# Optimization experiments

Measured on AMD Instinct MI355X. Metric: run time of the kernel, lower is better.

Reference implementation:

```python
import jax, jax.numpy as jnp
import numpy as np

B, T, C = 4, 2048, 1024
NH = 16
HD = C // NH
ROPE_BASE = 10000.0


def setup_inputs() -> dict:
    key = jax.random.key(0)
    k1, k2, k3, k4, k5 = jax.random.split(key, 5)
    s = 1.0 / np.sqrt(C)
    return {
        "x": jax.random.normal(k1, (B, T, C), dtype=jnp.float32),
        "W_qkv": jax.random.normal(k2, (C, 3 * C), dtype=jnp.float32) * s,
        "b_qkv": jax.random.normal(k3, (3 * C,), dtype=jnp.float32) * 0.02,
        "W_proj": jax.random.normal(k4, (C, C), dtype=jnp.float32) * s,
        "b_proj": jax.random.normal(k5, (C,), dtype=jnp.float32) * 0.02,
    }


def _rotate_half(u):
    u1, u2 = u[..., : HD // 2], u[..., HD // 2 :]
    return jnp.concatenate((-u2, u1), axis=-1)


def _rope_cos_sin(t, dtype):
    # inv_freq: [HD/2]; positions: [T]
    inv_freq = 1.0 / (ROPE_BASE ** (jnp.arange(0, HD, 2, dtype=jnp.float32) / HD))
    pos = jnp.arange(t, dtype=jnp.float32)
    freqs = pos[:, None] * inv_freq[None, :]          # [T, HD/2]
    emb = jnp.concatenate((freqs, freqs), axis=-1)    # [T, HD]
    return jnp.cos(emb).astype(dtype), jnp.sin(emb).astype(dtype)


def reference(x, W_qkv, b_qkv, W_proj, b_proj):
    b, t, c = x.shape
    qkv = x @ W_qkv + b_qkv                           # [B,T,3C]
    q, k, v = jnp.split(qkv, 3, axis=-1)
    # [B,T,C] -> [B,NH,T,HD]
    def to_heads(u):
        return u.reshape(b, t, NH, HD).transpose(0, 2, 1, 3)
    q, k, v = to_heads(q), to_heads(k), to_heads(v)
    cos, sin = _rope_cos_sin(t, x.dtype)              # [T,HD] each; broadcast over B,NH
    q = q * cos + _rotate_half(q) * sin
    k = k * cos + _rotate_half(k) * sin
    att = jnp.einsum("bhqd,bhkd->bhqk", q, k) * (1.0 / np.sqrt(HD))
    causal = jnp.tril(jnp.ones((t, t), dtype=bool))
    att = jnp.where(causal, att, -jnp.inf)
    att = jax.nn.softmax(att, axis=-1)
    y = jnp.einsum("bhqk,bhkd->bhqd", att, v)         # [B,NH,T,HD]
    y = y.transpose(0, 2, 1, 3).reshape(b, t, c)
    return y @ W_proj + b_proj
```

## Files before the change

kernel.cpp:

```cpp
#include <hip/hip_runtime.h>
#include <cstdint>
#include <cstddef>

typedef __attribute__((ext_vector_type(8))) short short8;
typedef __attribute__((ext_vector_type(4))) float float4x;

__device__ __forceinline__ uint16_t f2b(float f){
  uint32_t u = __builtin_bit_cast(uint32_t, f);
  u += 0x7FFFu + ((u >> 16) & 1u);
  return (uint16_t)(u >> 16);
}
__device__ __forceinline__ float b2f(uint16_t h){
  uint32_t u = ((uint32_t)h) << 16;
  return __builtin_bit_cast(float, u);
}
__device__ __forceinline__ float4x zero4(){
  float4x v; v[0]=0.f; v[1]=0.f; v[2]=0.f; v[3]=0.f; return v;
}
__device__ __forceinline__ void gload16(const uint16_t* g, uint16_t* l){
  __builtin_amdgcn_global_load_lds(
      (const __attribute__((address_space(1))) uint32_t*)g,
      (__attribute__((address_space(3))) uint32_t*)l, 16, 0, 0);
}

__global__ __launch_bounds__(256) void k_f32_to_bf16(const float* __restrict__ in,
                                                     uint16_t* __restrict__ out, int n4){
  int i = blockIdx.x * 256 + threadIdx.x;
  if (i < n4){
    float4 v = ((const float4*)in)[i];
    ushort4 o;
    o.x = f2b(v.x); o.y = f2b(v.y); o.z = f2b(v.z); o.w = f2b(v.w);
    ((ushort4*)out)[i] = o;
  }
}

__global__ __launch_bounds__(256) void k_transpose_bf16(const float* __restrict__ W,
                                                        uint16_t* __restrict__ Wt, int K, int N){
  __shared__ float tile[32][33];
  int k0 = blockIdx.y * 32, n0 = blockIdx.x * 32;
  int c = threadIdx.x & 31, r0 = threadIdx.x >> 5;
  for (int rr = r0; rr < 32; rr += 8)
    tile[rr][c] = W[(size_t)(k0 + rr) * N + n0 + c];
  __syncthreads();
  for (int rr = r0; rr < 32; rr += 8)
    Wt[(size_t)(n0 + rr) * K + k0 + c] = f2b(tile[c][rr]);
}

template<int OUTF>
__global__ __launch_bounds__(256, 3) void k_gemm_bt(const uint16_t* __restrict__ A,
                                                    const uint16_t* __restrict__ Bt,
                                                    const float* __restrict__ bias,
                                                    void* __restrict__ Cout,
                                                    int M, int N, int K){
  __shared__ __align__(16) uint16_t As[2][128*32];
  __shared__ __align__(16) uint16_t Bs[2][128*32];
  const int tid = threadIdx.x, lane = tid & 63, wave = tid >> 6;
  const int wr = wave >> 1, wc = wave & 1;
  const int m0 = blockIdx.y * 128, n0 = blockIdx.x * 128;
  const int quad = lane >> 4, l15 = lane & 15;
  const int rowA = tid >> 2, chA = tid & 3;

  float4x acc[4][4];
  for (int i = 0; i < 4; i++) for (int j = 0; j < 4; j++) acc[i][j] = zero4();

  const uint16_t* pa0 = &A[(size_t)(m0 + rowA)*K + chA*8];
  const uint16_t* pa1 = &A[(size_t)(m0 + rowA + 64)*K + chA*8];
  const uint16_t* pb0 = &Bt[(size_t)(n0 + rowA)*K + chA*8];
  const uint16_t* pb1 = &Bt[(size_t)(n0 + rowA + 64)*K + chA*8];

  gload16(pa0, &As[0][tid*8]);
  gload16(pa1, &As[0][64*32 + tid*8]);
  gload16(pb0, &Bs[0][tid*8]);
  gload16(pb1, &Bs[0][64*32 + tid*8]);

  int buf = 0;
  for (int k0 = 0; k0 < K; k0 += 32){
    __syncthreads();
    if (k0 + 32 < K){
      int nb = buf ^ 1;
      gload16(pa0 + k0 + 32, &As[nb][tid*8]);
      gload16(pa1 + k0 + 32, &As[nb][64*32 + tid*8]);
      gload16(pb0 + k0 + 32, &Bs[nb][tid*8]);
      gload16(pb1 + k0 + 32, &Bs[nb][64*32 + tid*8]);
    }
    short8 af[4], bf[4];
#pragma unroll
    for (int mt = 0; mt < 4; mt++)
      af[mt] = *(const short8*)&As[buf][(wr*64 + mt*16 + l15)*32 + quad*8];
#pragma unroll
    for (int nt = 0; nt < 4; nt++)
      bf[nt] = *(const short8*)&Bs[buf][(wc*64 + nt*16 + l15)*32 + quad*8];
#pragma unroll
    for (int mt = 0; mt < 4; mt++)
#pragma unroll
      for (int nt = 0; nt < 4; nt++)
        acc[mt][nt] = __builtin_amdgcn_mfma_f32_16x16x32_bf16(af[mt], bf[nt], acc[mt][nt], 0, 0, 0);
    buf ^= 1;
  }

#pragma unroll
  for (int mt = 0; mt < 4; mt++){
    int grow = m0 + wr*64 + mt*16 + quad*4;
#pragma unroll
    for (int nt = 0; nt < 4; nt++){
      int gcol = n0 + wc*64 + nt*16 + l15;
      float bv = bias[gcol];
#pragma unroll
      for (int r = 0; r < 4; r++){
        float v = acc[mt][nt][r] + bv;
        if (OUTF) ((float*)Cout)[(size_t)(grow + r)*N + gcol] = v;
        else      ((uint16_t*)Cout)[(size_t)(grow + r)*N + gcol] = f2b(v);
      }
    }
  }
}

__global__ __launch_bounds__(256) void k_rope(uint16_t* __restrict__ qkv){
  int idx = blockIdx.x * 256 + threadIdx.x;
  int i = idx & 31;
  int h = (idx >> 5) & 15;
  int t = (idx >> 9) & 2047;
  int b = (idx >> 20) & 3;
  int which = idx >> 22;
  size_t base = ((size_t)(b*2048 + t))*3072 + (size_t)which*1024 + h*64 + i;
  float u1 = b2f(qkv[base]), u2 = b2f(qkv[base + 32]);
  float inv = exp2f(-(float)i * 0.4152410118609203f);
  float ang = (float)t * inv;
  float s, c;
  __sincosf(ang, &s, &c);
  qkv[base]      = f2b(u1*c - u2*s);
  qkv[base + 32] = f2b(u2*c + u1*s);
}

__global__ __launch_bounds__(256) void k_transpose_v(const uint16_t* __restrict__ qkv,
                                                     uint16_t* __restrict__ vt){
  __shared__ __align__(16) uint16_t tile[64*72];
  int bh = blockIdx.y;
  int t0 = blockIdx.x * 64;
  int b = bh >> 4, h = bh & 15;
  int r = threadIdx.x >> 2, ch = threadIdx.x & 3;
  const uint16_t* src = &qkv[((size_t)(b*2048 + t0 + r))*3072 + 2048 + h*64];
  *(uint4*)&tile[r*72 + ch*8]      = *(const uint4*)&src[ch*8];
  *(uint4*)&tile[r*72 + 32 + ch*8] = *(const uint4*)&src[32 + ch*8];
  __syncthreads();
  short8 v0, v1;
#pragma unroll
  for (int j = 0; j < 8; j++) v0[j] = (short)tile[(ch*8 + j)*72 + r];
#pragma unroll
  for (int j = 0; j < 8; j++) v1[j] = (short)tile[(32 + ch*8 + j)*72 + r];
  uint16_t* dst = &vt[((size_t)(bh*64 + r))*2048 + t0];
  *(short8*)&dst[ch*8]      = v0;
  *(short8*)&dst[32 + ch*8] = v1;
}

__global__ __launch_bounds__(256) void k_attn(const uint16_t* __restrict__ qkv,
                                              const uint16_t* __restrict__ vt,
                                              uint16_t* __restrict__ y){
  __shared__ __align__(16) uint16_t Klds[2][64*64];
  __shared__ __align__(16) uint16_t Vlds[2][64*64];
  __shared__ __align__(16) uint16_t Ps[4*32*72];

  const int Did = blockIdx.x;
  const int g = Did & 7, ii = Did >> 3;
  const int bh = g*8 + (ii >> 3);
  const int X  = ii & 7;
  const int b = bh >> 4, h = bh & 15;
  const int lane = threadIdx.x & 63, w = threadIdx.x >> 6;
  const int quad = lane >> 4, l15 = lane & 15;
  const int swz = l15 & 7;
  uint16_t* Pw = &Ps[w*32*72];

  const uint16_t* Qbase  = qkv + (size_t)b*2048*3072 + h*64;
  const uint16_t* Kbase  = qkv + (size_t)b*2048*3072 + 1024 + h*64;
  const uint16_t* Vtbase = vt  + (size_t)bh*64*2048;
  const float M = 30.0f;

  const int isV  = w >> 1;
  const int rbase = (w & 1) * 32;
  const int rsub = lane >> 3, csub = lane & 7;

  const int cA = X, cB = 15 - X;
  const int KT_A = 2*cA + 2;
  const int TS = 34;

  int c = cA;
  int qrow0 = c*128 + w*32;

  short8 aq[2][2];
#pragma unroll
  for (int mt = 0; mt < 2; mt++)
#pragma unroll
    for (int hf = 0; hf < 2; hf++)
      aq[mt][hf] = *(const short8*)&Qbase[(size_t)(qrow0 + mt*16 + l15)*3072 + hf*32 + quad*8];

  float4x o[2][4];
#pragma unroll
  for (int mt = 0; mt < 2; mt++) for (int nt = 0; nt < 4; nt++) o[mt][nt] = zero4();
  float lrow[2][4];
#pragma unroll
  for (int mt = 0; mt < 2; mt++) for (int rr = 0; rr < 4; rr++) lrow[mt][rr] = 0.f;

  auto epilogue = [&](){
#pragma unroll
    for (int mt = 0; mt < 2; mt++)
#pragma unroll
      for (int rr = 0; rr < 4; rr++){
        float sm = lrow[mt][rr];
        for (int d = 1; d < 16; d <<= 1) sm += __shfl_xor(sm, d);
        float linv = 1.f / sm;
        int tq = qrow0 + mt*16 + quad*4 + rr;
        size_t rowbase = ((size_t)(b*2048 + tq))*1024 + h*64;
#pragma unroll
        for (int nt = 0; nt < 4; nt++)
          y[rowbase + nt*16 + l15] = f2b(o[mt][nt][rr] * linv);
      }
  };

#pragma unroll
  for (int j = 0; j < 4; j++){
    int r  = rbase + j*8 + rsub;
    int cg = csub ^ (r & 7);
    if (isV) gload16(Vtbase + (size_t)r*2048 + cg*8, &Vlds[0][(rbase + j*8)*64 + lane*8]);
    else     gload16(Kbase  + (size_t)r*3072 + cg*8, &Klds[0][(rbase + j*8)*64 + lane*8]);
  }

  int cur = 0;
  for (int t = 0; t < TS; ++t){
    __syncthreads();
    const int kt = (t < KT_A) ? t : t - KT_A;
    if (t + 1 < TS){
      const int ktn = (t + 1 < KT_A) ? t + 1 : t + 1 - KT_A;
      int nb = cur ^ 1;
#pragma unroll
      for (int j = 0; j < 4; j++){
        int r  = rbase + j*8 + rsub;
        int cg = csub ^ (r & 7);
        if (isV) gload16(Vtbase + (size_t)r*2048 + (size_t)ktn*64 + cg*8,
                         &Vlds[nb][(rbase + j*8)*64 + lane*8]);
        else     gload16(Kbase  + (size_t)(ktn*64 + r)*3072 + cg*8,
                         &Klds[nb][(rbase + j*8)*64 + lane*8]);
      }
    }

    if (t == KT_A){
      epilogue();
      c = cB; qrow0 = c*128 + w*32;
#pragma unroll
      for (int mt = 0; mt < 2; mt++)
#pragma unroll
        for (int hf = 0; hf < 2; hf++)
          aq[mt][hf] = *(const short8*)&Qbase[(size_t)(qrow0 + mt*16 + l15)*3072 + hf*32 + quad*8];
#pragma unroll
      for (int mt = 0; mt < 2; mt++) for (int nt = 0; nt < 4; nt++) o[mt][nt] = zero4();
#pragma unroll
      for (int mt = 0; mt < 2; mt++) for (int rr = 0; rr < 4; rr++) lrow[mt][rr] = 0.f;
    }

    float4x s[2][4];
#pragma unroll
    for (int mt = 0; mt < 2; mt++) for (int nt = 0; nt < 4; nt++) s[mt][nt] = zero4();
    __builtin_amdgcn_s_setprio(1);
#pragma unroll
    for (int nt = 0; nt < 4; nt++){
      const uint16_t* krow = &Klds[cur][(nt*16 + l15)*64];
      short8 bk0 = *(const short8*)&krow[(quad ^ swz)*8];
      short8 bk1 = *(const short8*)&krow[((4 + quad) ^ swz)*8];
      s[0][nt] = __builtin_amdgcn_mfma_f32_16x16x32_bf16(aq[0][0], bk0, s[0][nt], 0, 0, 0);
      s[1][nt] = __builtin_amdgcn_mfma_f32_16x16x32_bf16(aq[1][0], bk0, s[1][nt], 0, 0, 0);
      s[0][nt] = __builtin_amdgcn_mfma_f32_16x16x32_bf16(aq[0][1], bk1, s[0][nt], 0, 0, 0);
      s[1][nt] = __builtin_amdgcn_mfma_f32_16x16x32_bf16(aq[1][1], bk1, s[1][nt], 0, 0, 0);
    }
    __builtin_amdgcn_s_setprio(0);

    if (kt >= 2*c){
#pragma unroll
      for (int mt = 0; mt < 2; mt++)
#pragma unroll
        for (int nt = 0; nt < 4; nt++)
#pragma unroll
          for (int rr = 0; rr < 4; rr++){
            int tk = kt*64 + nt*16 + l15;
            int tq = qrow0 + mt*16 + quad*4 + rr;
            if (tk > tq) s[mt][nt][rr] = -1e30f;
          }
    }

#pragma unroll
    for (int mt = 0; mt < 2; mt++)
#pragma unroll
      for (int nt = 0; nt < 4; nt++)
#pragma unroll
        for (int rr = 0; rr < 4; rr++){
          float pv = __expf(__builtin_fmaf(s[mt][nt][rr], 0.125f, -M));
          lrow[mt][rr] += pv;
          Pw[(mt*16 + quad*4 + rr)*72 + nt*16 + l15] = f2b(pv);
        }

    short8 ap[2][2];
#pragma unroll
    for (int mt = 0; mt < 2; mt++){
      ap[mt][0] = *(const short8*)&Pw[(mt*16 + l15)*72 + quad*8];
      ap[mt][1] = *(const short8*)&Pw[(mt*16 + l15)*72 + 32 + quad*8];
    }
    __builtin_amdgcn_s_setprio(1);
#pragma unroll
    for (int nt = 0; nt < 4; nt++){
      const uint16_t* vrow = &Vlds[cur][(nt*16 + l15)*64];
      short8 bv0 = *(const short8*)&vrow[(quad ^ swz)*8];
      short8 bv1 = *(const short8*)&vrow[((4 + quad) ^ swz)*8];
      o[0][nt] = __builtin_amdgcn_mfma_f32_16x16x32_bf16(ap[0][0], bv0, o[0][nt], 0, 0, 0);
      o[1][nt] = __builtin_amdgcn_mfma_f32_16x16x32_bf16(ap[1][0], bv0, o[1][nt], 0, 0, 0);
      o[0][nt] = __builtin_amdgcn_mfma_f32_16x16x32_bf16(ap[0][1], bv1, o[0][nt], 0, 0, 0);
      o[1][nt] = __builtin_amdgcn_mfma_f32_16x16x32_bf16(ap[1][1], bv1, o[1][nt], 0, 0, 0);
    }
    __builtin_amdgcn_s_setprio(0);
    cur ^= 1;
  }

  epilogue();
}

extern "C" void kernel_launch(void* const* d_in, const int* in_sizes, int n_in,
                              void* d_out, int out_size, void* d_ws, size_t ws_size,
                              hipStream_t stream){
  const float* x     = (const float*)d_in[0];
  const float* Wqkv  = (const float*)d_in[1];
  const float* bqkv  = (const float*)d_in[2];
  const float* Wproj = (const float*)d_in[3];
  const float* bproj = (const float*)d_in[4];

  uint16_t* p = (uint16_t*)d_ws;
  uint16_t* xb    = p; p += (size_t)8192*1024;
  uint16_t* wqkvt = p; p += (size_t)3072*1024;
  uint16_t* wprjt = p; p += (size_t)1024*1024;
  uint16_t* qkv   = p; p += (size_t)8192*3072;
  uint16_t* vt    = p; p += (size_t)64*64*2048;
  uint16_t* yb    = p; p += (size_t)8192*1024;

  k_f32_to_bf16<<<8192, 256, 0, stream>>>(x, xb, 2097152);
  k_transpose_bf16<<<dim3(96, 32), 256, 0, stream>>>(Wqkv, wqkvt, 1024, 3072);
  k_transpose_bf16<<<dim3(32, 32), 256, 0, stream>>>(Wproj, wprjt, 1024, 1024);
  k_gemm_bt<0><<<dim3(24, 64), 256, 0, stream>>>(xb, wqkvt, bqkv, (void*)qkv, 8192, 3072, 1024);
  k_rope<<<32768, 256, 0, stream>>>(qkv);
  k_transpose_v<<<dim3(32, 64), 256, 0, stream>>>(qkv, vt);
  k_attn<<<512, 256, 0, stream>>>(qkv, vt, yb);
  k_gemm_bt<1><<<dim3(8, 64), 256, 0, stream>>>(yb, wprjt, bproj, d_out, 8192, 1024, 1024);
}
```

Before: 290.8 us.

## Switch attention to 32x32 MFMA with transposed S and register-resident P

```diff
diff --git a/kernel.cpp b/kernel.cpp
--- a/kernel.cpp
+++ b/kernel.cpp
@@ -4,6 +4,8 @@
 
 typedef __attribute__((ext_vector_type(8))) short short8;
 typedef __attribute__((ext_vector_type(4))) float float4x;
+typedef __attribute__((ext_vector_type(16))) float float16x;
+typedef __attribute__((ext_vector_type(2))) unsigned int uint2v;
 
 __device__ __forceinline__ uint16_t f2b(float f){
   uint32_t u = __builtin_bit_cast(uint32_t, f);
@@ -16,6 +18,37 @@
 }
 __device__ __forceinline__ float4x zero4(){
   float4x v; v[0]=0.f; v[1]=0.f; v[2]=0.f; v[3]=0.f; return v;
+}
+__device__ __forceinline__ float16x zero16(){
+  float16x v;
+#pragma unroll
+  for (int i = 0; i < 16; i++) v[i] = 0.f;
+  return v;
+}
+__device__ __forceinline__ uint32_t cvtpk(float lo, float hi){
+  uint32_t r;
+  asm("v_cvt_pk_bf16_f32 %0, %1, %2" : "=v"(r) : "v"(lo), "v"(hi));
+  return r;
+}
+__device__ __forceinline__ void plswap(uint32_t &a, uint32_t &b){
+#if __has_builtin(__builtin_amdgcn_permlane32_swap)
+  uint2v r = __builtin_amdgcn_permlane32_swap(a, b, false, false);
+  a = r[0]; b = r[1];
+#else
+  uint32_t a2 = (uint32_t)__shfl_xor((int)a, 32, 64);
+  uint32_t b2 = (uint32_t)__shfl_xor((int)b, 32, 64);
+  bool lo = ((threadIdx.x & 63) < 32);
+  uint32_t an = lo ? a : b2;
+  uint32_t bn = lo ? a2 : b;
+  a = an; b = bn;
+#endif
+}
+__device__ __forceinline__ float fexp2(float x){
+#if __has_builtin(__builtin_amdgcn_exp2f)
+  return __builtin_amdgcn_exp2f(x);
+#else
+  return exp2f(x);
+#endif
 }
 __device__ __forceinline__ void gload16(const uint16_t* g, uint16_t* l){
   __builtin_amdgcn_global_load_lds(
@@ -158,7 +191,6 @@
                                               uint16_t* __restrict__ y){
   __shared__ __align__(16) uint16_t Klds[2][64*64];
   __shared__ __align__(16) uint16_t Vlds[2][64*64];
-  __shared__ __align__(16) uint16_t Ps[4*32*72];
 
   const int Did = blockIdx.x;
   const int g = Did & 7, ii = Did >> 3;
@@ -166,14 +198,14 @@
   const int X  = ii & 7;
   const int b = bh >> 4, h = bh & 15;
   const int lane = threadIdx.x & 63, w = threadIdx.x >> 6;
-  const int quad = lane >> 4, l15 = lane & 15;
-  const int swz = l15 & 7;
-  uint16_t* Pw = &Ps[w*32*72];
+  const int l31 = lane & 31, hi = lane >> 5;
 
   const uint16_t* Qbase  = qkv + (size_t)b*2048*3072 + h*64;
   const uint16_t* Kbase  = qkv + (size_t)b*2048*3072 + 1024 + h*64;
   const uint16_t* Vtbase = vt  + (size_t)bh*64*2048;
-  const float M = 30.0f;
+
+  const float S2 = 0.18033688011112042f;
+  const float M2 = 43.28085122666890f;
 
   const int isV  = w >> 1;
   const int rbase = (w & 1) * 32;
@@ -184,35 +216,31 @@
   const int TS = 34;
 
   int c = cA;
-  int qrow0 = c*128 + w*32;
-
-  short8 aq[2][2];
-#pragma unroll
-  for (int mt = 0; mt < 2; mt++)
-#pragma unroll
-    for (int hf = 0; hf < 2; hf++)
-      aq[mt][hf] = *(const short8*)&Qbase[(size_t)(qrow0 + mt*16 + l15)*3072 + hf*32 + quad*8];
-
-  float4x o[2][4];
-#pragma unroll
-  for (int mt = 0; mt < 2; mt++) for (int nt = 0; nt < 4; nt++) o[mt][nt] = zero4();
-  float lrow[2][4];
-#pragma unroll
-  for (int mt = 0; mt < 2; mt++) for (int rr = 0; rr < 4; rr++) lrow[mt][rr] = 0.f;
+  int qr = c*128 + w*32;
+
+  short8 aq[4];
+#pragma unroll
+  for (int kc = 0; kc < 4; kc++)
+    aq[kc] = *(const short8*)&Qbase[(size_t)(qr + l31)*3072 + kc*16 + hi*8];
+
+  float16x o[2];
+  o[0] = zero16(); o[1] = zero16();
+  float lr4[4] = {0.f, 0.f, 0.f, 0.f};
 
   auto epilogue = [&](){
-#pragma unroll
-    for (int mt = 0; mt < 2; mt++)
-#pragma unroll
-      for (int rr = 0; rr < 4; rr++){
-        float sm = lrow[mt][rr];
-        for (int d = 1; d < 16; d <<= 1) sm += __shfl_xor(sm, d);
-        float linv = 1.f / sm;
-        int tq = qrow0 + mt*16 + quad*4 + rr;
-        size_t rowbase = ((size_t)(b*2048 + tq))*1024 + h*64;
-#pragma unroll
-        for (int nt = 0; nt < 4; nt++)
-          y[rowbase + nt*16 + l15] = f2b(o[mt][nt][rr] * linv);
+    float l = (lr4[0] + lr4[1]) + (lr4[2] + lr4[3]);
+    l += __shfl_xor(l, 32, 64);
+    float linv = 1.f / l;
+    float lv[16];
+#pragma unroll
+    for (int r = 0; r < 16; r++)
+      lv[r] = __shfl(linv, (r&3) + 8*(r>>2) + 4*hi, 64);
+#pragma unroll
+    for (int dt = 0; dt < 2; dt++)
+#pragma unroll
+      for (int r = 0; r < 16; r++){
+        int row = (r&3) + 8*(r>>2) + 4*hi;
+        y[((size_t)(b*2048 + qr + row))*1024 + h*64 + dt*32 + l31] = f2b(o[dt][r] * lv[r]);
       }
   };
 
@@ -244,74 +272,66 @@
 
     if (t == KT_A){
       epilogue();
-      c = cB; qrow0 = c*128 + w*32;
-#pragma unroll
-      for (int mt = 0; mt < 2; mt++)
-#pragma unroll
-        for (int hf = 0; hf < 2; hf++)
-          aq[mt][hf] = *(const short8*)&Qbase[(size_t)(qrow0 + mt*16 + l15)*3072 + hf*32 + quad*8];
-#pragma unroll
-      for (int mt = 0; mt < 2; mt++) for (int nt = 0; nt < 4; nt++) o[mt][nt] = zero4();
-#pragma unroll
-      for (int mt = 0; mt < 2; mt++) for (int rr = 0; rr < 4; rr++) lrow[mt][rr] = 0.f;
-    }
-
-    float4x s[2][4];
-#pragma unroll
-    for (int mt = 0; mt < 2; mt++) for (int nt = 0; nt < 4; nt++) s[mt][nt] = zero4();
+      c = cB; qr = c*128 + w*32;
+#pragma unroll
+      for (int kc = 0; kc < 4; kc++)
+        aq[kc] = *(const short8*)&Qbase[(size_t)(qr + l31)*3072 + kc*16 + hi*8];
+      o[0] = zero16(); o[1] = zero16();
+      lr4[0] = lr4[1] = lr4[2] = lr4[3] = 0.f;
+    }
+
+    float16x p0 = zero16(), p1 = zero16();
     __builtin_amdgcn_s_setprio(1);
 #pragma unroll
-    for (int nt = 0; nt < 4; nt++){
-      const uint16_t* krow = &Klds[cur][(nt*16 + l15)*64];
-      short8 bk0 = *(const short8*)&krow[(quad ^ swz)*8];
-      short8 bk1 = *(const short8*)&krow[((4 + quad) ^ swz)*8];
-      s[0][nt] = __builtin_amdgcn_mfma_f32_16x16x32_bf16(aq[0][0], bk0, s[0][nt], 0, 0, 0);
-      s[1][nt] = __builtin_amdgcn_mfma_f32_16x16x32_bf16(aq[1][0], bk0, s[1][nt], 0, 0, 0);
-      s[0][nt] = __builtin_amdgcn_mfma_f32_16x16x32_bf16(aq[0][1], bk1, s[0][nt], 0, 0, 0);
-      s[1][nt] = __builtin_amdgcn_mfma_f32_16x16x32_bf16(aq[1][1], bk1, s[1][nt], 0, 0, 0);
+    for (int kc = 0; kc < 4; kc++){
+      const int ch = 2*kc + hi;
+      short8 ak0 = *(const short8*)&Klds[cur][(l31)*64      + ((ch ^ (l31 & 7))*8)];
+      short8 ak1 = *(const short8*)&Klds[cur][(32 + l31)*64 + ((ch ^ (l31 & 7))*8)];
+      p0 = __builtin_amdgcn_mfma_f32_32x32x16_bf16(ak0, aq[kc], p0, 0, 0, 0);
+      p1 = __builtin_amdgcn_mfma_f32_32x32x16_bf16(ak1, aq[kc], p1, 0, 0, 0);
     }
     __builtin_amdgcn_s_setprio(0);
 
     if (kt >= 2*c){
-#pragma unroll
-      for (int mt = 0; mt < 2; mt++)
-#pragma unroll
-        for (int nt = 0; nt < 4; nt++)
-#pragma unroll
-          for (int rr = 0; rr < 4; rr++){
-            int tk = kt*64 + nt*16 + l15;
-            int tq = qrow0 + mt*16 + quad*4 + rr;
-            if (tk > tq) s[mt][nt][rr] = -1e30f;
-          }
-    }
-
-#pragma unroll
-    for (int mt = 0; mt < 2; mt++)
-#pragma unroll
-      for (int nt = 0; nt < 4; nt++)
-#pragma unroll
-        for (int rr = 0; rr < 4; rr++){
-          float pv = __expf(__builtin_fmaf(s[mt][nt][rr], 0.125f, -M));
-          lrow[mt][rr] += pv;
-          Pw[(mt*16 + quad*4 + rr)*72 + nt*16 + l15] = f2b(pv);
-        }
-
-    short8 ap[2][2];
-#pragma unroll
-    for (int mt = 0; mt < 2; mt++){
-      ap[mt][0] = *(const short8*)&Pw[(mt*16 + l15)*72 + quad*8];
-      ap[mt][1] = *(const short8*)&Pw[(mt*16 + l15)*72 + 32 + quad*8];
-    }
+      const int tq = qr + l31;
+#pragma unroll
+      for (int r = 0; r < 16; r++){
+        int kb = kt*64 + (r&3) + 8*(r>>2) + 4*hi;
+        if (kb > tq)      p0[r] = -1e30f;
+        if (kb + 32 > tq) p1[r] = -1e30f;
+      }
+    }
+
+#pragma unroll
+    for (int r = 0; r < 16; r++){
+      float e0 = fexp2(__builtin_fmaf(p0[r], S2, -M2));
+      float e1 = fexp2(__builtin_fmaf(p1[r], S2, -M2));
+      lr4[r & 3] += e0 + e1;
+      p0[r] = e0; p1[r] = e1;
+    }
+
     __builtin_amdgcn_s_setprio(1);
 #pragma unroll
-    for (int nt = 0; nt < 4; nt++){
-      const uint16_t* vrow = &Vlds[cur][(nt*16 + l15)*64];
-      short8 bv0 = *(const short8*)&vrow[(quad ^ swz)*8];
-      short8 bv1 = *(const short8*)&vrow[((4 + quad) ^ swz)*8];
-      o[0][nt] = __builtin_amdgcn_mfma_f32_16x16x32_bf16(ap[0][0], bv0, o[0][nt], 0, 0, 0);
-      o[1][nt] = __builtin_amdgcn_mfma_f32_16x16x32_bf16(ap[1][0], bv0, o[1][nt], 0, 0, 0);
-      o[0][nt] = __builtin_amdgcn_mfma_f32_16x16x32_bf16(ap[0][1], bv1, o[0][nt], 0, 0, 0);
-      o[1][nt] = __builtin_amdgcn_mfma_f32_16x16x32_bf16(ap[1][1], bv1, o[1][nt], 0, 0, 0);
+    for (int kc = 0; kc < 4; kc++){
+      const int e8 = (kc & 1)*8;
+      uint32_t w0, w1, w2, w3;
+      if (kc < 2){
+        w0 = cvtpk(p0[e8+0], p0[e8+1]); w1 = cvtpk(p0[e8+2], p0[e8+3]);
+        w2 = cvtpk(p0[e8+4], p0[e8+5]); w3 = cvtpk(p0[e8+6], p0[e8+7]);
+      } else {
+        w0 = cvtpk(p1[e8+0], p1[e8+1]); w1 = cvtpk(p1[e8+2], p1[e8+3]);
+        w2 = cvtpk(p1[e8+4], p1[e8+5]); w3 = cvtpk(p1[e8+6], p1[e8+7]);
+      }
+      plswap(w0, w2);
+      plswap(w1, w3);
+      union { uint32_t u[4]; short8 s; } ap;
+      ap.u[0] = w0; ap.u[1] = w1; ap.u[2] = w2; ap.u[3] = w3;
+
+      const int ch = 2*kc + hi;
+      short8 bv0 = *(const short8*)&Vlds[cur][(l31)*64      + ((ch ^ (l31 & 7))*8)];
+      short8 bv1 = *(const short8*)&Vlds[cur][(32 + l31)*64 + ((ch ^ (l31 & 7))*8)];
+      o[0] = __builtin_amdgcn_mfma_f32_32x32x16_bf16(ap.s, bv0, o[0], 0, 0, 0);
+      o[1] = __builtin_amdgcn_mfma_f32_32x32x16_bf16(ap.s, bv1, o[1], 0, 0, 0);
     }
     __builtin_amdgcn_s_setprio(0);
     cur ^= 1;
```

Measured after the change: 283.2 us. 2.6% less time.
